# Optimization experiments

Hardware: AMD Instinct MI355X
Metric: run time of the kernel (lower is better)

Reference implementation:

```python
import jax, jax.numpy as jnp
import numpy as np

N = 20000      # nodes
E = 120000     # directed edges (self-loops added in reference, per PyG default)
F_IN = 235
HID = 256
HEADS = 8
NEG_SLOPE = 0.2


def setup_inputs() -> dict:
    key = jax.random.key(0)
    ks = jax.random.split(key, 24)
    p = lambda k, shape: (jax.random.normal(k, shape, jnp.float32) * 0.05)
    inp = {}
    inp["x"] = jax.random.normal(ks[0], (N, F_IN), jnp.float32)
    inp["edge_index"] = jax.random.randint(ks[1], (2, E), 0, N, jnp.int32)
    # input projection
    inp["w_in"] = p(ks[2], (F_IN, HID)); inp["b_in"] = jnp.zeros((HID,), jnp.float32)
    # temporal MLP
    inp["w_t1"] = p(ks[3], (HID, HID)); inp["b_t1"] = jnp.zeros((HID,), jnp.float32)
    inp["w_t2"] = p(ks[4], (HID, HID)); inp["b_t2"] = jnp.zeros((HID,), jnp.float32)
    # GAT layer 1: heads=8, out_per_head=32, concat -> 256
    C1 = HID // HEADS
    inp["w_g1"] = p(ks[5], (HID, HEADS * C1)); inp["a_src1"] = p(ks[6], (HEADS, C1))
    inp["a_dst1"] = p(ks[7], (HEADS, C1)); inp["b_g1"] = jnp.zeros((HEADS * C1,), jnp.float32)
    # GAT layer 2: same shape
    inp["w_g2"] = p(ks[8], (HID, HEADS * C1)); inp["a_src2"] = p(ks[9], (HEADS, C1))
    inp["a_dst2"] = p(ks[10], (HEADS, C1)); inp["b_g2"] = jnp.zeros((HEADS * C1,), jnp.float32)
    # GAT layer 3: heads=8, out_per_head=256, concat -> 2048
    inp["w_g3"] = p(ks[11], (HID, HEADS * HID)); inp["a_src3"] = p(ks[12], (HEADS, HID))
    inp["a_dst3"] = p(ks[13], (HEADS, HID)); inp["b_g3"] = jnp.zeros((HEADS * HID,), jnp.float32)
    # classifier
    inp["w_c1"] = p(ks[14], (2 * HID, HID)); inp["b_c1"] = jnp.zeros((HID,), jnp.float32)
    inp["w_c2"] = p(ks[15], (HID, 2)); inp["b_c2"] = jnp.zeros((2,), jnp.float32)
    return inp


def _gat(x, src, dst, W, a_src, a_dst, b, C):
    """PyG-style GATConv: gather -> per-edge logits -> segment softmax -> scatter-add."""
    h = (x @ W).reshape(-1, HEADS, C)                       # [N, H, C]
    alpha_s = jnp.sum(h * a_src, axis=-1)                   # [N, H]
    alpha_d = jnp.sum(h * a_dst, axis=-1)                   # [N, H]
    e = jax.nn.leaky_relu(alpha_s[src] + alpha_d[dst], NEG_SLOPE)   # [Etot, H]
    m = jax.ops.segment_max(e, dst, num_segments=N)         # [N, H] (self-loops ensure non-empty)
    ex = jnp.exp(e - m[dst])
    den = jax.ops.segment_sum(ex, dst, num_segments=N)
    alpha = ex / (den[dst] + 1e-16)                          # [Etot, H]
    out = jax.ops.segment_sum(alpha[:, :, None] * h[src], dst, num_segments=N)  # [N, H, C]
    return out.reshape(-1, HEADS * C) + b


def reference(x, edge_index, w_in, b_in, w_t1, b_t1, w_t2, b_t2,
              w_g1, a_src1, a_dst1, b_g1, w_g2, a_src2, a_dst2, b_g2,
              w_g3, a_src3, a_dst3, b_g3, w_c1, b_c1, w_c2, b_c2):
    h = jax.nn.elu(x @ w_in + b_in)                          # [N, 256]
    t = jax.nn.relu(h @ w_t1 + b_t1) @ w_t2 + b_t2          # [N, 256] (dropout inactive in eval)
    loop = jnp.arange(N, dtype=edge_index.dtype)
    src = jnp.concatenate([edge_index[0], loop])
    dst = jnp.concatenate([edge_index[1], loop])
    g = jax.nn.elu(_gat(h, src, dst, w_g1, a_src1, a_dst1, b_g1, HID // HEADS))
    g = jax.nn.elu(_gat(g, src, dst, w_g2, a_src2, a_dst2, b_g2, HID // HEADS))
    g = jax.nn.elu(_gat(g, src, dst, w_g3, a_src3, a_dst3, b_g3, HID))  # [N, 2048]
    g = g.reshape(N, HEADS, HID).mean(axis=1)                # [N, 256]
    comb = jnp.concatenate([g, t], axis=-1)                  # [N, 512]
    logits = jax.nn.relu(comb @ w_c1 + b_c1) @ w_c2 + b_c2   # [N, 2]
    return logits
```

## Files before the change

### kernel.cpp

```cpp
#include <hip/hip_runtime.h>
#include <hip/hip_bf16.h>
#include <math.h>


#define HID 256
#define HEADS 8
#define FIN 235

typedef __attribute__((ext_vector_type(8))) short short8;
typedef __attribute__((ext_vector_type(4))) float floatx4;

__device__ __forceinline__ float elu_f(float x) { return x > 0.f ? x : __expf(x) - 1.f; }
__device__ __forceinline__ float bf2f(unsigned short u) {
  return __uint_as_float(((unsigned int)u) << 16);
}
__device__ __forceinline__ unsigned short f2bfu(float f) {
  union { __hip_bfloat16 b; unsigned short u; } c;
  c.b = __float2bfloat16(f);
  return c.u;
}

__global__ void xcvt_k(const float* __restrict__ x, __hip_bfloat16* __restrict__ xb, int M) {
  int id = blockIdx.x * blockDim.x + threadIdx.x;
  if (id >= M * 256) return;
  int m = id >> 8, k = id & 255;
  xb[id] = (k < FIN) ? __float2bfloat16(x[(size_t)m * FIN + k]) : __float2bfloat16(0.f);
}

__global__ void wprep_k(const float* __restrict__ w_in, const float* __restrict__ w_t1,
                        const float* __restrict__ w_g1, const float* __restrict__ w_t2,
                        const float* __restrict__ w_g2, const float* __restrict__ w_c1,
                        const float* __restrict__ w_g3, __hip_bfloat16* __restrict__ wtin,
                        __hip_bfloat16* __restrict__ wtpair, __hip_bfloat16* __restrict__ wtt2,
                        __hip_bfloat16* __restrict__ wtg2, __hip_bfloat16* __restrict__ wtc1,
                        __hip_bfloat16* __restrict__ wtg3s) {
  __shared__ float t[32][33];
  int z = blockIdx.z;
  const float* src;
  __hip_bfloat16* dst;
  int K, Kpad, Nstride;
  if (z == 5) {
    src = w_c1; dst = wtc1; K = 512; Kpad = 512; Nstride = 256;
  } else {
    if (blockIdx.y >= 8) return;
    switch (z) {
      case 0: src = w_in; dst = wtin; K = FIN; Kpad = 256; Nstride = 256; break;
      case 1: src = w_t1; dst = wtpair; K = 256; Kpad = 256; Nstride = 256; break;
      case 2: src = w_g1; dst = wtpair + 256 * 256; K = 256; Kpad = 256; Nstride = 256; break;
      case 3: src = w_t2; dst = wtt2; K = 256; Kpad = 256; Nstride = 256; break;
      case 4: src = w_g2; dst = wtg2; K = 256; Kpad = 256; Nstride = 256; break;
      default: {
        int h = z - 6;
        src = w_g3 + h * 256; dst = wtg3s + h * 256; K = 256; Kpad = 2048; Nstride = 2048;
      }
    }
  }
  int nb = blockIdx.x * 32, kb = blockIdx.y * 32;
  int tx = threadIdx.x, ty = threadIdx.y;
#pragma unroll
  for (int j = 0; j < 32; j += 8) {
    int k = kb + ty + j;
    t[ty + j][tx] = (k < K) ? src[(size_t)k * Nstride + nb + tx] : 0.f;
  }
  __syncthreads();
#pragma unroll
  for (int j = 0; j < 32; j += 8) {
    int n = nb + ty + j;
    int k = kb + tx;
    dst[(size_t)n * Kpad + k] = __float2bfloat16(t[tx][ty + j]);
  }
}

__global__ void count_k(const int* __restrict__ ei, int* __restrict__ deg, int E) {
  int i = blockIdx.x * blockDim.x + threadIdx.x;
  if (i < E) atomicAdd(&deg[ei[E + i]], 1);
}

__global__ void scan_k(const int* __restrict__ deg, int* __restrict__ rp, int n) {
  __shared__ int wsum[16];
  __shared__ int s_carry;
  int tid = threadIdx.x, lane = tid & 63, wid = tid >> 6;
  if (tid == 0) { s_carry = 0; rp[0] = 0; }
  __syncthreads();
  for (int base = 0; base < n; base += 1024) {
    int i = base + tid;
    int x = (i < n) ? (deg[i] + 1) : 0;
#pragma unroll
    for (int off = 1; off < 64; off <<= 1) {
      int y = __shfl_up(x, off);
      if (lane >= off) x += y;
    }
    if (lane == 63) wsum[wid] = x;
    __syncthreads();
    if (wid == 0 && lane < 16) {
      int s = wsum[lane];
#pragma unroll
      for (int off = 1; off < 16; off <<= 1) {
        int y = __shfl_up(s, off);
        if (lane >= off) s += y;
      }
      wsum[lane] = s;
    }
    __syncthreads();
    int offset = s_carry + (wid > 0 ? wsum[wid - 1] : 0);
    if (i < n) rp[i + 1] = offset + x;
    __syncthreads();
    if (tid == 1023) s_carry += wsum[15];
    __syncthreads();
  }
}

__global__ void fill_k(const int* __restrict__ ei, const int* __restrict__ rp,
                       int* __restrict__ fillc, int* __restrict__ colA, int E, int n) {
  int i = blockIdx.x * blockDim.x + threadIdx.x;
  if (i < E) {
    int d = ei[E + i];
    int pos = rp[d] + atomicAdd(&fillc[d], 1);
    colA[pos] = ei[i];
  } else if (i < E + n) {
    int v = i - E;
    int pos = rp[v] + atomicAdd(&fillc[v], 1);
    colA[pos] = v;
  }
}

template <int ACT>
__global__ __launch_bounds__(256) void mgemm64_k(
    const __hip_bfloat16* __restrict__ A, const __hip_bfloat16* __restrict__ Bt,
    const float* __restrict__ bias, __hip_bfloat16* __restrict__ Cb,
    int ldc, int M, int N, int K) {
  __shared__ short As[64 * 40];
  __shared__ short Bs[64 * 40];
  int tid = threadIdx.x;
  int row0 = blockIdx.y * 64, col0 = blockIdx.x * 64;
  int w = tid >> 6, lane = tid & 63;
  int wr = w >> 1, wc = w & 1;
  int quad = lane >> 4, l16 = lane & 15;
  floatx4 zero = {0.f, 0.f, 0.f, 0.f};
  floatx4 acc[2][2];
#pragma unroll
  for (int i = 0; i < 2; i++)
#pragma unroll
    for (int j = 0; j < 2; j++) acc[i][j] = zero;

  int srow = tid >> 2, sq = tid & 3;
  const __hip_bfloat16* Ap = A + (size_t)(row0 + srow) * K + sq * 8;
  const __hip_bfloat16* Bp = Bt + (size_t)(col0 + srow) * K + sq * 8;
  bool aok = (row0 + srow) < M;

  uint4 a1 = make_uint4(0, 0, 0, 0);
  if (aok) a1 = *(const uint4*)(Ap);
  uint4 b1 = *(const uint4*)(Bp);

  for (int k0 = 0; k0 < K; k0 += 32) {
    __syncthreads();
    *(uint4*)&As[srow * 40 + sq * 8] = a1;
    *(uint4*)&Bs[srow * 40 + sq * 8] = b1;
    int kn = k0 + 32;
    if (kn < K) {
      if (aok) a1 = *(const uint4*)(Ap + kn);
      b1 = *(const uint4*)(Bp + kn);
    }
    __syncthreads();
    short8 fa[2], fb[2];
#pragma unroll
    for (int i = 0; i < 2; i++) {
      fa[i] = *(const short8*)&As[(wr * 32 + i * 16 + l16) * 40 + quad * 8];
      fb[i] = *(const short8*)&Bs[(wc * 32 + i * 16 + l16) * 40 + quad * 8];
    }
#pragma unroll
    for (int mi = 0; mi < 2; mi++)
#pragma unroll
      for (int ni = 0; ni < 2; ni++)
        acc[mi][ni] = __builtin_amdgcn_mfma_f32_16x16x32_bf16(fa[mi], fb[ni], acc[mi][ni], 0, 0, 0);
  }

#pragma unroll
  for (int mi = 0; mi < 2; mi++) {
    int rbase = row0 + wr * 32 + mi * 16 + quad * 4;
#pragma unroll
    for (int ni = 0; ni < 2; ni++) {
      int c = col0 + wc * 32 + ni * 16 + l16;
      float bv = bias ? bias[c] : 0.f;
#pragma unroll
      for (int reg = 0; reg < 4; reg++) {
        int rr = rbase + reg;
        if (rr >= M) continue;
        float v = acc[mi][ni][reg] + bv;
        if (ACT == 1) v = fmaxf(v, 0.f);
        if (ACT == 2) v = elu_f(v);
        Cb[(size_t)rr * ldc + c] = __float2bfloat16(v);
      }
    }
  }
}

__global__ __launch_bounds__(256) void mgemm_dual_k(
    const __hip_bfloat16* __restrict__ A, const __hip_bfloat16* __restrict__ Bt,
    const float* __restrict__ bias1, __hip_bfloat16* __restrict__ O1,
    __hip_bfloat16* __restrict__ O2, int M) {
  const int K = 256;
  __shared__ short As[64 * 40];
  __shared__ short Bs[128 * 40];
  int tid = threadIdx.x;
  int row0 = blockIdx.y * 64, col0 = blockIdx.x * 128;
  int w = tid >> 6, lane = tid & 63;
  int wr = w >> 1, wc = w & 1;
  int quad = lane >> 4, l16 = lane & 15;
  floatx4 zero = {0.f, 0.f, 0.f, 0.f};
  floatx4 acc[2][4];
#pragma unroll
  for (int i = 0; i < 2; i++)
#pragma unroll
    for (int j = 0; j < 4; j++) acc[i][j] = zero;

  int srow = tid >> 2, sq = tid & 3;
  const __hip_bfloat16* Ap = A + (size_t)(row0 + srow) * K + sq * 8;
  const __hip_bfloat16* Bp1 = Bt + (size_t)(col0 + srow) * K + sq * 8;
  const __hip_bfloat16* Bp2 = Bt + (size_t)(col0 + 64 + srow) * K + sq * 8;
  bool aok = (row0 + srow) < M;

  uint4 a1 = make_uint4(0, 0, 0, 0);
  if (aok) a1 = *(const uint4*)(Ap);
  uint4 b1 = *(const uint4*)(Bp1);
  uint4 b2 = *(const uint4*)(Bp2);

  for (int k0 = 0; k0 < K; k0 += 32) {
    __syncthreads();
    *(uint4*)&As[srow * 40 + sq * 8] = a1;
    *(uint4*)&Bs[srow * 40 + sq * 8] = b1;
    *(uint4*)&Bs[(64 + srow) * 40 + sq * 8] = b2;
    int kn = k0 + 32;
    if (kn < K) {
      if (aok) a1 = *(const uint4*)(Ap + kn);
      b1 = *(const uint4*)(Bp1 + kn);
      b2 = *(const uint4*)(Bp2 + kn);
    }
    __syncthreads();
    short8 fa[2], fb[4];
#pragma unroll
    for (int i = 0; i < 2; i++)
      fa[i] = *(const short8*)&As[(wr * 32 + i * 16 + l16) * 40 + quad * 8];
#pragma unroll
    for (int i = 0; i < 4; i++)
      fb[i] = *(const short8*)&Bs[(wc * 64 + i * 16 + l16) * 40 + quad * 8];
#pragma unroll
    for (int mi = 0; mi < 2; mi++)
#pragma unroll
      for (int ni = 0; ni < 4; ni++)
        acc[mi][ni] = __builtin_amdgcn_mfma_f32_16x16x32_bf16(fa[mi], fb[ni], acc[mi][ni], 0, 0, 0);
  }

#pragma unroll
  for (int mi = 0; mi < 2; mi++) {
    int rbase = row0 + wr * 32 + mi * 16 + quad * 4;
#pragma unroll
    for (int ni = 0; ni < 4; ni++) {
      int c = col0 + wc * 64 + ni * 16 + l16;
      bool first = c < 256;
      float bv = first ? bias1[c] : 0.f;
      int cc = first ? c : (c - 256);
#pragma unroll
      for (int reg = 0; reg < 4; reg++) {
        int rr = rbase + reg;
        if (rr >= M) continue;
        float v = acc[mi][ni][reg] + bv;
        if (first) v = fmaxf(v, 0.f);
        __hip_bfloat16* dst = first ? O1 : O2;
        dst[(size_t)rr * 256 + cc] = __float2bfloat16(v);
      }
    }
  }
}

__global__ __launch_bounds__(256) void mgemm3_k(
    const __hip_bfloat16* __restrict__ A, const __hip_bfloat16* __restrict__ Bt,
    const float* __restrict__ bias, __hip_bfloat16* __restrict__ comb, int M) {
  const int K = 2048;
  __shared__ short As[64 * 40];
  __shared__ short Bs[64 * 40];
  int tid = threadIdx.x;
  int row0 = blockIdx.y * 64, col0 = blockIdx.x * 64;
  int w = tid >> 6, lane = tid & 63;
  int wr = w >> 1, wc = w & 1;
  int quad = lane >> 4, l16 = lane & 15;
  floatx4 zero = {0.f, 0.f, 0.f, 0.f};
  floatx4 acc[2][2], sum[2][2];
#pragma unroll
  for (int i = 0; i < 2; i++)
#pragma unroll
    for (int j = 0; j < 2; j++) { acc[i][j] = zero; sum[i][j] = zero; }

  int srow = tid >> 2, sq = tid & 3;
  const __hip_bfloat16* Ap = A + (size_t)(row0 + srow) * K + sq * 8;
  const __hip_bfloat16* Bp = Bt + (size_t)(col0 + srow) * K + sq * 8;
  bool aok = (row0 + srow) < M;

  uint4 a1 = make_uint4(0, 0, 0, 0);
  if (aok) a1 = *(const uint4*)(Ap);
  uint4 b1 = *(const uint4*)(Bp);

  for (int k0 = 0; k0 < K; k0 += 32) {
    __syncthreads();
    *(uint4*)&As[srow * 40 + sq * 8] = a1;
    *(uint4*)&Bs[srow * 40 + sq * 8] = b1;
    int kn = k0 + 32;
    if (kn < K) {
      if (aok) a1 = *(const uint4*)(Ap + kn);
      b1 = *(const uint4*)(Bp + kn);
    }
    __syncthreads();
    short8 fa[2], fb[2];
#pragma unroll
    for (int i = 0; i < 2; i++) {
      fa[i] = *(const short8*)&As[(wr * 32 + i * 16 + l16) * 40 + quad * 8];
      fb[i] = *(const short8*)&Bs[(wc * 32 + i * 16 + l16) * 40 + quad * 8];
    }
#pragma unroll
    for (int mi = 0; mi < 2; mi++)
#pragma unroll
      for (int ni = 0; ni < 2; ni++)
        acc[mi][ni] = __builtin_amdgcn_mfma_f32_16x16x32_bf16(fa[mi], fb[ni], acc[mi][ni], 0, 0, 0);
    if (((k0 + 32) & 255) == 0) {
      int h = k0 >> 8;
#pragma unroll
      for (int mi = 0; mi < 2; mi++)
#pragma unroll
        for (int ni = 0; ni < 2; ni++) {
          int c = col0 + wc * 32 + ni * 16 + l16;
          float bv = bias[h * 256 + c];
#pragma unroll
          for (int reg = 0; reg < 4; reg++) {
            sum[mi][ni][reg] += elu_f(acc[mi][ni][reg] + bv);
            acc[mi][ni][reg] = 0.f;
          }
        }
    }
  }

#pragma unroll
  for (int mi = 0; mi < 2; mi++) {
    int rbase = row0 + wr * 32 + mi * 16 + quad * 4;
#pragma unroll
    for (int ni = 0; ni < 2; ni++) {
      int c = col0 + wc * 32 + ni * 16 + l16;
#pragma unroll
      for (int reg = 0; reg < 4; reg++) {
        int rr = rbase + reg;
        if (rr >= M) continue;
        comb[(size_t)rr * 512 + c] = __float2bfloat16(sum[mi][ni][reg] * 0.125f);
      }
    }
  }
}

__global__ __launch_bounds__(256) void mgemm_cls_k(
    const __hip_bfloat16* __restrict__ A, const __hip_bfloat16* __restrict__ Bt,
    const float* __restrict__ bias, const float* __restrict__ w2,
    float* __restrict__ out, int M) {
  const int K = 512;
  __shared__ short As[64 * 40];
  __shared__ short Bs[64 * 40];
  __shared__ float ls[64][2][2];
  int tid = threadIdx.x;
  int row0 = blockIdx.y * 64, col0 = blockIdx.x * 64;
  int w = tid >> 6, lane = tid & 63;
  int wr = w >> 1, wc = w & 1;
  int quad = lane >> 4, l16 = lane & 15;
  floatx4 zero = {0.f, 0.f, 0.f, 0.f};
  floatx4 acc[2][2];
#pragma unroll
  for (int i = 0; i < 2; i++)
#pragma unroll
    for (int j = 0; j < 2; j++) acc[i][j] = zero;

  int srow = tid >> 2, sq = tid & 3;
  const __hip_bfloat16* Ap = A + (size_t)(row0 + srow) * K + sq * 8;
  const __hip_bfloat16* Bp = Bt + (size_t)(col0 + srow) * K + sq * 8;
  bool aok = (row0 + srow) < M;

  uint4 a1 = make_uint4(0, 0, 0, 0);
  if (aok) a1 = *(const uint4*)(Ap);
  uint4 b1 = *(const uint4*)(Bp);

  for (int k0 = 0; k0 < K; k0 += 32) {
    __syncthreads();
    *(uint4*)&As[srow * 40 + sq * 8] = a1;
    *(uint4*)&Bs[srow * 40 + sq * 8] = b1;
    int kn = k0 + 32;
    if (kn < K) {
      if (aok) a1 = *(const uint4*)(Ap + kn);
      b1 = *(const uint4*)(Bp + kn);
    }
    __syncthreads();
    short8 fa[2], fb[2];
#pragma unroll
    for (int i = 0; i < 2; i++) {
      fa[i] = *(const short8*)&As[(wr * 32 + i * 16 + l16) * 40 + quad * 8];
      fb[i] = *(const short8*)&Bs[(wc * 32 + i * 16 + l16) * 40 + quad * 8];
    }
#pragma unroll
    for (int mi = 0; mi < 2; mi++)
#pragma unroll
      for (int ni = 0; ni < 2; ni++)
        acc[mi][ni] = __builtin_amdgcn_mfma_f32_16x16x32_bf16(fa[mi], fb[ni], acc[mi][ni], 0, 0, 0);
  }

  float p[2][4][2];
#pragma unroll
  for (int mi = 0; mi < 2; mi++)
#pragma unroll
    for (int reg = 0; reg < 4; reg++) { p[mi][reg][0] = 0.f; p[mi][reg][1] = 0.f; }
#pragma unroll
  for (int mi = 0; mi < 2; mi++) {
    int rbase = row0 + wr * 32 + mi * 16 + quad * 4;
#pragma unroll
    for (int ni = 0; ni < 2; ni++) {
      int c = col0 + wc * 32 + ni * 16 + l16;
      float bv = bias[c];
      float w20 = w2[c * 2 + 0], w21 = w2[c * 2 + 1];
#pragma unroll
      for (int reg = 0; reg < 4; reg++) {
        if (rbase + reg >= M) continue;
        float v = fmaxf(acc[mi][ni][reg] + bv, 0.f);
        p[mi][reg][0] += v * w20;
        p[mi][reg][1] += v * w21;
      }
    }
  }
#pragma unroll
  for (int off = 1; off < 16; off <<= 1)
#pragma unroll
    for (int mi = 0; mi < 2; mi++)
#pragma unroll
      for (int reg = 0; reg < 4; reg++) {
        p[mi][reg][0] += __shfl_xor(p[mi][reg][0], off);
        p[mi][reg][1] += __shfl_xor(p[mi][reg][1], off);
      }
  if (l16 == 0) {
#pragma unroll
    for (int mi = 0; mi < 2; mi++)
#pragma unroll
      for (int reg = 0; reg < 4; reg++) {
        int rl = wr * 32 + mi * 16 + quad * 4 + reg;
        ls[rl][wc][0] = p[mi][reg][0];
        ls[rl][wc][1] = p[mi][reg][1];
      }
  }
  __syncthreads();
  if (tid < 64) {
    int r = row0 + tid;
    if (r < M) {
      atomicAdd(&out[r * 2 + 0], ls[tid][0][0] + ls[tid][1][0]);
      atomicAdd(&out[r * 2 + 1], ls[tid][0][1] + ls[tid][1][1]);
    }
  }
}

__global__ void initout_k(const float* __restrict__ b, float* __restrict__ out, int M) {
  int i = blockIdx.x * blockDim.x + threadIdx.x;
  if (i < M * 2) out[i] = b[i & 1];
}

__global__ void aproj_k(const float* __restrict__ w_g3, const float* __restrict__ a_s,
                        const float* __restrict__ a_d, float* __restrict__ apj) {
  int idx = blockIdx.x * blockDim.x + threadIdx.x;
  if (idx >= 256 * 16) return;
  int k = idx >> 4, o = idx & 15;
  int h = o >> 1;
  const float* av = (o & 1) ? (a_d + h * 256) : (a_s + h * 256);
  const float* wr = w_g3 + (size_t)k * 2048 + h * 256;
  float s = 0.f;
  for (int c = 0; c < 256; c++) s += wr[c] * av[c];
  apj[idx] = s;
}

__global__ __launch_bounds__(256) void alpha3_k(const __hip_bfloat16* __restrict__ g2,
                                                const float* __restrict__ apj,
                                                float* __restrict__ as_, float* __restrict__ ad_,
                                                int M) {
  int tid = threadIdx.x;
  int nl = tid >> 4, o = tid & 15;
  int n = blockIdx.x * 16 + nl;
  if (n >= M) return;
  const __hip_bfloat16* row = g2 + (size_t)n * 256;
  float s = 0.f;
  for (int c = 0; c < 256; c++) s += __bfloat162float(row[c]) * apj[c * 16 + o];
  if (o & 1) ad_[n * 8 + (o >> 1)] = s;
  else as_[n * 8 + (o >> 1)] = s;
}

__global__ void alpha_small_k(const __hip_bfloat16* __restrict__ hW, const float* __restrict__ a_s,
                              const float* __restrict__ a_d, float* __restrict__ as_,
                              float* __restrict__ ad_, int M) {
  int idx = blockIdx.x * blockDim.x + threadIdx.x;
  if (idx >= M * HEADS) return;
  int h = idx & 7;
  const __hip_bfloat16* row = hW + (size_t)(idx >> 3) * HID + h * 32;
  const float* ws = a_s + h * 32;
  const float* wd = a_d + h * 32;
  float s = 0.f, d = 0.f;
#pragma unroll
  for (int c = 0; c < 32; c++) {
    float v = __bfloat162float(row[c]);
    s += v * ws[c];
    d += v * wd[c];
  }
  as_[idx] = s;
  ad_[idx] = d;
}

__global__ __launch_bounds__(256) void aggf_k(const int* __restrict__ rp,
                                              const int* __restrict__ col,
                                              const __hip_bfloat16* __restrict__ hW,
                                              const float* __restrict__ as_,
                                              const float* __restrict__ ad_,
                                              const float* __restrict__ bias,
                                              __hip_bfloat16* __restrict__ out, int M) {
  int dst = blockIdx.x * 4 + (threadIdx.x >> 6);
  if (dst >= M) return;
  int t = threadIdx.x & 63;
  int h = t >> 3, c = t << 2;
  int beg = rp[dst], end = rp[dst + 1];
  float adv = ad_[dst * 8 + h];
  float m = -3.4e38f;
  for (int i = beg; i < end; i++) {
    float e = as_[col[i] * 8 + h] + adv;
    e = e > 0.f ? e : 0.2f * e;
    m = fmaxf(m, e);
  }
  float den = 0.f;
  float a0 = 0.f, a1 = 0.f, a2 = 0.f, a3 = 0.f;
  for (int i = beg; i < end; i++) {
    int s = col[i];
    float e = as_[s * 8 + h] + adv;
    e = e > 0.f ? e : 0.2f * e;
    float ex = __expf(e - m);
    den += ex;
    union { uint2 u; unsigned short us[4]; } uu;
    uu.u = *(const uint2*)(hW + (size_t)s * HID + c);
    a0 += ex * bf2f(uu.us[0]);
    a1 += ex * bf2f(uu.us[1]);
    a2 += ex * bf2f(uu.us[2]);
    a3 += ex * bf2f(uu.us[3]);
  }
  float inv = 1.f / (den + 1e-16f);
  out[(size_t)dst * HID + c + 0] = __float2bfloat16(elu_f(a0 * inv + bias[c + 0]));
  out[(size_t)dst * HID + c + 1] = __float2bfloat16(elu_f(a1 * inv + bias[c + 1]));
  out[(size_t)dst * HID + c + 2] = __float2bfloat16(elu_f(a2 * inv + bias[c + 2]));
  out[(size_t)dst * HID + c + 3] = __float2bfloat16(elu_f(a3 * inv + bias[c + 3]));
}

__global__ __launch_bounds__(256) void esoft_k(const int* __restrict__ rp,
                                               const int* __restrict__ col,
                                               const float* __restrict__ as_,
                                               const float* __restrict__ ad_,
                                               float* __restrict__ ex,
                                               float* __restrict__ invden, int M) {
  int dst = blockIdx.x * 4 + (threadIdx.x >> 6);
  if (dst >= M) return;
  int lane = threadIdx.x & 63;
  int es = lane >> 3, h = lane & 7;
  int beg = rp[dst], end = rp[dst + 1];
  float adv = ad_[dst * 8 + h];
  float m = -3.4e38f;
  for (int i = beg + es; i < end; i += 8) {
    float e = as_[col[i] * 8 + h] + adv;
    e = e > 0.f ? e : 0.2f * e;
    m = fmaxf(m, e);
  }
  m = fmaxf(m, __shfl_xor(m, 8));
  m = fmaxf(m, __shfl_xor(m, 16));
  m = fmaxf(m, __shfl_xor(m, 32));
  float den = 0.f;
  for (int i = beg + es; i < end; i += 8) {
    float e = as_[col[i] * 8 + h] + adv;
    e = e > 0.f ? e : 0.2f * e;
    float v = __expf(e - m);
    ex[(size_t)i * 8 + h] = v;
    den += v;
  }
  den += __shfl_xor(den, 8);
  den += __shfl_xor(den, 16);
  den += __shfl_xor(den, 32);
  if (es == 0) invden[dst * 8 + h] = 1.f / (den + 1e-16f);
}

__global__ __launch_bounds__(256) void agg3_k(const int* __restrict__ rp,
                                              const int* __restrict__ col,
                                              const __hip_bfloat16* __restrict__ g2,
                                              const float* __restrict__ ex,
                                              const float* __restrict__ invden,
                                              __hip_bfloat16* __restrict__ outA, int M) {
  int dst = blockIdx.x * 2 + (threadIdx.x >> 7);
  if (dst >= M) return;
  int t = threadIdx.x & 127;
  int beg = rp[dst], end = rp[dst + 1];
  float acc0[8] = {}, acc1[8] = {};
  for (int i = beg; i < end; i++) {
    int s = col[i];
    float4 w0 = *(const float4*)(ex + (size_t)i * 8);
    float4 w1 = *(const float4*)(ex + (size_t)i * 8 + 4);
    union { unsigned int u; unsigned short us[2]; } uu;
    uu.u = *(const unsigned int*)(g2 + (size_t)s * 256 + t * 2);
    float v0 = bf2f(uu.us[0]), v1 = bf2f(uu.us[1]);
    acc0[0] += w0.x * v0; acc0[1] += w0.y * v0; acc0[2] += w0.z * v0; acc0[3] += w0.w * v0;
    acc0[4] += w1.x * v0; acc0[5] += w1.y * v0; acc0[6] += w1.z * v0; acc0[7] += w1.w * v0;
    acc1[0] += w0.x * v1; acc1[1] += w0.y * v1; acc1[2] += w0.z * v1; acc1[3] += w0.w * v1;
    acc1[4] += w1.x * v1; acc1[5] += w1.y * v1; acc1[6] += w1.z * v1; acc1[7] += w1.w * v1;
  }
#pragma unroll
  for (int h = 0; h < 8; h++) {
    float inv = invden[dst * 8 + h];
    unsigned int pack = (unsigned int)f2bfu(acc0[h] * inv) |
                        ((unsigned int)f2bfu(acc1[h] * inv) << 16);
    *(unsigned int*)(outA + (size_t)dst * 2048 + h * 256 + t * 2) = pack;
  }
}

extern "C" void kernel_launch(void* const* d_in, const int* in_sizes, int n_in,
                              void* d_out, int out_size, void* d_ws, size_t ws_size,
                              hipStream_t stream) {
  const float* x      = (const float*)d_in[0];
  const int*   ei     = (const int*)d_in[1];
  const float* w_in   = (const float*)d_in[2];
  const float* b_in   = (const float*)d_in[3];
  const float* w_t1   = (const float*)d_in[4];
  const float* b_t1   = (const float*)d_in[5];
  const float* w_t2   = (const float*)d_in[6];
  const float* b_t2   = (const float*)d_in[7];
  const float* w_g1   = (const float*)d_in[8];
  const float* a_src1 = (const float*)d_in[9];
  const float* a_dst1 = (const float*)d_in[10];
  const float* b_g1   = (const float*)d_in[11];
  const float* w_g2   = (const float*)d_in[12];
  const float* a_src2 = (const float*)d_in[13];
  const float* a_dst2 = (const float*)d_in[14];
  const float* b_g2   = (const float*)d_in[15];
  const float* w_g3   = (const float*)d_in[16];
  const float* a_src3 = (const float*)d_in[17];
  const float* a_dst3 = (const float*)d_in[18];
  const float* b_g3   = (const float*)d_in[19];
  const float* w_c1   = (const float*)d_in[20];
  const float* b_c1   = (const float*)d_in[21];
  const float* w_c2   = (const float*)d_in[22];
  const float* b_c2   = (const float*)d_in[23];
  const int M = in_sizes[0] / FIN;
  const int E = in_sizes[1] / 2;
  (void)n_in; (void)out_size; (void)ws_size;

  char* wsb = (char*)d_ws;
  size_t off = 0;
  auto alloc = [&](size_t bytes) {
    void* p = wsb + off;
    off = (off + bytes + 255) & ~(size_t)255;
    return p;
  };
  typedef __hip_bfloat16 bf;
  bf* xb     = (bf*)alloc((size_t)M * 256 * 2);
  bf* wtin   = (bf*)alloc(256 * 256 * 2);
  bf* wtpair = (bf*)alloc(512 * 256 * 2);
  bf* wtt2   = (bf*)alloc(256 * 256 * 2);
  bf* wtg2   = (bf*)alloc(256 * 256 * 2);
  bf* wtg3s  = (bf*)alloc(256 * 2048 * 2);
  bf* wtc1   = (bf*)alloc(256 * 512 * 2);
  bf* actA   = (bf*)alloc((size_t)M * HID * 2);
  bf* actB   = (bf*)alloc((size_t)M * HID * 2);
  bf* hW1    = (bf*)alloc((size_t)M * HID * 2);
  bf* comb   = (bf*)alloc((size_t)M * 2 * HID * 2);
  bf* hWb    = (bf*)alloc((size_t)M * 2048 * 2);
  float* as_ = (float*)alloc((size_t)M * 8 * 4);
  float* ad_ = (float*)alloc((size_t)M * 8 * 4);
  float* apj = (float*)alloc(256 * 16 * 4);
  float* exw = (float*)alloc((size_t)(E + M) * 8 * 4);
  float* ivd = (float*)alloc((size_t)M * 8 * 4);
  int* degfill = (int*)alloc((size_t)2 * M * 4);
  int* deg   = degfill;
  int* fillc = degfill + M;
  int* rp    = (int*)alloc((size_t)(M + 1) * 4);
  int* colA  = (int*)alloc((size_t)(E + M) * 4);

  xcvt_k<<<(M * 256 + 255) / 256, 256, 0, stream>>>(x, xb, M);
  wprep_k<<<dim3(8, 16, 14), dim3(32, 8), 0, stream>>>(
      w_in, w_t1, w_g1, w_t2, w_g2, w_c1, w_g3, wtin, wtpair, wtt2, wtg2, wtc1, wtg3s);
  aproj_k<<<16, 256, 0, stream>>>(w_g3, a_src3, a_dst3, apj);

  hipMemsetAsync(degfill, 0, (size_t)2 * M * 4, stream);
  count_k<<<(E + 255) / 256, 256, 0, stream>>>(ei, deg, E);
  scan_k<<<1, 1024, 0, stream>>>(deg, rp, M);
  fill_k<<<(E + M + 255) / 256, 256, 0, stream>>>(ei, rp, fillc, colA, E, M);

  int eg = (M + 3) / 4;
  int mg = (M + 63) / 64;

  mgemm64_k<2><<<dim3(4, mg), 256, 0, stream>>>(xb, wtin, b_in, actA, HID, M, HID, 256);
  mgemm_dual_k<<<dim3(4, mg), 256, 0, stream>>>(actA, wtpair, b_t1, actB, hW1, M);
  mgemm64_k<0><<<dim3(4, mg), 256, 0, stream>>>(actB, wtt2, b_t2, comb + HID, 2 * HID, M, HID, 256);

  alpha_small_k<<<(M * 8 + 255) / 256, 256, 0, stream>>>(hW1, a_src1, a_dst1, as_, ad_, M);
  aggf_k<<<eg, 256, 0, stream>>>(rp, colA, hW1, as_, ad_, b_g1, actB, M);

  mgemm64_k<0><<<dim3(4, mg), 256, 0, stream>>>(actB, wtg2, nullptr, hW1, HID, M, HID, 256);
  alpha_small_k<<<(M * 8 + 255) / 256, 256, 0, stream>>>(hW1, a_src2, a_dst2, as_, ad_, M);
  aggf_k<<<eg, 256, 0, stream>>>(rp, colA, hW1, as_, ad_, b_g2, actA, M);

  alpha3_k<<<(M + 15) / 16, 256, 0, stream>>>(actA, apj, as_, ad_, M);
  esoft_k<<<eg, 256, 0, stream>>>(rp, colA, as_, ad_, exw, ivd, M);
  agg3_k<<<(M + 1) / 2, 256, 0, stream>>>(rp, colA, actA, exw, ivd, hWb, M);
  mgemm3_k<<<dim3(4, mg), 256, 0, stream>>>(hWb, wtg3s, b_g3, comb, M);

  initout_k<<<(M * 2 + 255) / 256, 256, 0, stream>>>(b_c2, (float*)d_out, M);
  mgemm_cls_k<<<dim3(4, mg), 256, 0, stream>>>(comb, wtc1, b_c1, w_c2, (float*)d_out, M);
}
```

Measured before the change: 446.6 us.

## Widen GEMM tiles to full width, drop atomics, vectorize alpha and aggregation loads

mgemm3 and the classifier GEMM now run 512-thread blocks that each cover a 64-row by 256-column tile. A row's A tile is loaded once instead of four times, and the classifier writes its logits directly with the bias instead of using atomics and a separate init kernel. The a_src3/a_dst3 projection is folded into the weight-prep launch, and alpha3 caches the projection in shared memory and uses 16-byte row loads. agg3 handles four channels per thread with 8-byte loads. In exchange, each block uses more registers and shared memory and there are fewer blocks in flight.

```diff
diff --git a/kernel.cpp b/kernel.cpp
--- a/kernel.cpp
+++ b/kernel.cpp
@@ -30,12 +30,26 @@
 __global__ void wprep_k(const float* __restrict__ w_in, const float* __restrict__ w_t1,
                         const float* __restrict__ w_g1, const float* __restrict__ w_t2,
                         const float* __restrict__ w_g2, const float* __restrict__ w_c1,
-                        const float* __restrict__ w_g3, __hip_bfloat16* __restrict__ wtin,
+                        const float* __restrict__ w_g3, const float* __restrict__ a_s3,
+                        const float* __restrict__ a_d3, __hip_bfloat16* __restrict__ wtin,
                         __hip_bfloat16* __restrict__ wtpair, __hip_bfloat16* __restrict__ wtt2,
                         __hip_bfloat16* __restrict__ wtg2, __hip_bfloat16* __restrict__ wtc1,
-                        __hip_bfloat16* __restrict__ wtg3s) {
+                        __hip_bfloat16* __restrict__ wtg3s, float* __restrict__ apj) {
   __shared__ float t[32][33];
   int z = blockIdx.z;
+  if (z == 14) {
+    int idx = (blockIdx.y * 8 + blockIdx.x) * 256 + threadIdx.y * 32 + threadIdx.x;
+    if (idx < 256 * 16) {
+      int k = idx >> 4, o = idx & 15;
+      int h = o >> 1;
+      const float* av = (o & 1) ? (a_d3 + h * 256) : (a_s3 + h * 256);
+      const float* wr = w_g3 + (size_t)k * 2048 + h * 256;
+      float s = 0.f;
+      for (int c = 0; c < 256; c++) s += wr[c] * av[c];
+      apj[idx] = s;
+    }
+    return;
+  }
   const float* src;
   __hip_bfloat16* dst;
   int K, Kpad, Nstride;
@@ -273,219 +287,188 @@
   }
 }
 
-__global__ __launch_bounds__(256) void mgemm3_k(
+__global__ __launch_bounds__(512) void mgemm3_k(
     const __hip_bfloat16* __restrict__ A, const __hip_bfloat16* __restrict__ Bt,
     const float* __restrict__ bias, __hip_bfloat16* __restrict__ comb, int M) {
   const int K = 2048;
   __shared__ short As[64 * 40];
-  __shared__ short Bs[64 * 40];
+  __shared__ short Bs[256 * 40];
   int tid = threadIdx.x;
-  int row0 = blockIdx.y * 64, col0 = blockIdx.x * 64;
+  int row0 = blockIdx.x * 64;
   int w = tid >> 6, lane = tid & 63;
-  int wr = w >> 1, wc = w & 1;
+  int wr = w & 3, wc = w >> 2;
   int quad = lane >> 4, l16 = lane & 15;
-  floatx4 zero = {0.f, 0.f, 0.f, 0.f};
-  floatx4 acc[2][2], sum[2][2];
-#pragma unroll
-  for (int i = 0; i < 2; i++)
-#pragma unroll
-    for (int j = 0; j < 2; j++) { acc[i][j] = zero; sum[i][j] = zero; }
-
-  int srow = tid >> 2, sq = tid & 3;
-  const __hip_bfloat16* Ap = A + (size_t)(row0 + srow) * K + sq * 8;
-  const __hip_bfloat16* Bp = Bt + (size_t)(col0 + srow) * K + sq * 8;
-  bool aok = (row0 + srow) < M;
+  floatx4 acc[8], sum[8];
+#pragma unroll
+  for (int i = 0; i < 8; i++) {
+    acc[i] = (floatx4){0.f, 0.f, 0.f, 0.f};
+    sum[i] = (floatx4){0.f, 0.f, 0.f, 0.f};
+  }
+
+  bool at = tid < 256;
+  int arow = tid >> 2, achk = (tid & 3) * 8;
+  const __hip_bfloat16* Ap = A + (size_t)(row0 + arow) * K + achk;
+  bool aok = at && (row0 + arow) < M;
+  int brow = tid >> 1, boff = (tid & 1) * 16;
+  const __hip_bfloat16* Bp = Bt + (size_t)brow * K + boff;
 
   uint4 a1 = make_uint4(0, 0, 0, 0);
   if (aok) a1 = *(const uint4*)(Ap);
   uint4 b1 = *(const uint4*)(Bp);
+  uint4 b2 = *(const uint4*)(Bp + 8);
 
   for (int k0 = 0; k0 < K; k0 += 32) {
     __syncthreads();
-    *(uint4*)&As[srow * 40 + sq * 8] = a1;
-    *(uint4*)&Bs[srow * 40 + sq * 8] = b1;
+    if (at) *(uint4*)&As[arow * 40 + achk] = a1;
+    *(uint4*)&Bs[brow * 40 + boff] = b1;
+    *(uint4*)&Bs[brow * 40 + boff + 8] = b2;
     int kn = k0 + 32;
     if (kn < K) {
       if (aok) a1 = *(const uint4*)(Ap + kn);
       b1 = *(const uint4*)(Bp + kn);
-    }
-    __syncthreads();
-    short8 fa[2], fb[2];
-#pragma unroll
-    for (int i = 0; i < 2; i++) {
-      fa[i] = *(const short8*)&As[(wr * 32 + i * 16 + l16) * 40 + quad * 8];
-      fb[i] = *(const short8*)&Bs[(wc * 32 + i * 16 + l16) * 40 + quad * 8];
-    }
-#pragma unroll
-    for (int mi = 0; mi < 2; mi++)
-#pragma unroll
-      for (int ni = 0; ni < 2; ni++)
-        acc[mi][ni] = __builtin_amdgcn_mfma_f32_16x16x32_bf16(fa[mi], fb[ni], acc[mi][ni], 0, 0, 0);
+      b2 = *(const uint4*)(Bp + kn + 8);
+    }
+    __syncthreads();
+    short8 fa = *(const short8*)&As[(wr * 16 + l16) * 40 + quad * 8];
+#pragma unroll
+    for (int ni = 0; ni < 8; ni++) {
+      short8 fb = *(const short8*)&Bs[(wc * 128 + ni * 16 + l16) * 40 + quad * 8];
+      acc[ni] = __builtin_amdgcn_mfma_f32_16x16x32_bf16(fa, fb, acc[ni], 0, 0, 0);
+    }
     if (((k0 + 32) & 255) == 0) {
       int h = k0 >> 8;
 #pragma unroll
-      for (int mi = 0; mi < 2; mi++)
-#pragma unroll
-        for (int ni = 0; ni < 2; ni++) {
-          int c = col0 + wc * 32 + ni * 16 + l16;
-          float bv = bias[h * 256 + c];
-#pragma unroll
-          for (int reg = 0; reg < 4; reg++) {
-            sum[mi][ni][reg] += elu_f(acc[mi][ni][reg] + bv);
-            acc[mi][ni][reg] = 0.f;
-          }
+      for (int ni = 0; ni < 8; ni++) {
+        int c = wc * 128 + ni * 16 + l16;
+        float bv = bias[h * 256 + c];
+#pragma unroll
+        for (int reg = 0; reg < 4; reg++) {
+          sum[ni][reg] += elu_f(acc[ni][reg] + bv);
+          acc[ni][reg] = 0.f;
         }
-    }
-  }
-
-#pragma unroll
-  for (int mi = 0; mi < 2; mi++) {
-    int rbase = row0 + wr * 32 + mi * 16 + quad * 4;
-#pragma unroll
-    for (int ni = 0; ni < 2; ni++) {
-      int c = col0 + wc * 32 + ni * 16 + l16;
-#pragma unroll
-      for (int reg = 0; reg < 4; reg++) {
-        int rr = rbase + reg;
-        if (rr >= M) continue;
-        comb[(size_t)rr * 512 + c] = __float2bfloat16(sum[mi][ni][reg] * 0.125f);
       }
     }
   }
-}
-
-__global__ __launch_bounds__(256) void mgemm_cls_k(
+
+  int rbase = row0 + wr * 16 + quad * 4;
+#pragma unroll
+  for (int ni = 0; ni < 8; ni++) {
+    int c = wc * 128 + ni * 16 + l16;
+#pragma unroll
+    for (int reg = 0; reg < 4; reg++) {
+      int rr = rbase + reg;
+      if (rr >= M) continue;
+      comb[(size_t)rr * 512 + c] = __float2bfloat16(sum[ni][reg] * 0.125f);
+    }
+  }
+}
+
+__global__ __launch_bounds__(512) void mgemm_cls_k(
     const __hip_bfloat16* __restrict__ A, const __hip_bfloat16* __restrict__ Bt,
     const float* __restrict__ bias, const float* __restrict__ w2,
-    float* __restrict__ out, int M) {
+    const float* __restrict__ b2f, float* __restrict__ out, int M) {
   const int K = 512;
   __shared__ short As[64 * 40];
-  __shared__ short Bs[64 * 40];
+  __shared__ short Bs[256 * 40];
   __shared__ float ls[64][2][2];
   int tid = threadIdx.x;
-  int row0 = blockIdx.y * 64, col0 = blockIdx.x * 64;
+  int row0 = blockIdx.x * 64;
   int w = tid >> 6, lane = tid & 63;
-  int wr = w >> 1, wc = w & 1;
+  int wr = w & 3, wc = w >> 2;
   int quad = lane >> 4, l16 = lane & 15;
-  floatx4 zero = {0.f, 0.f, 0.f, 0.f};
-  floatx4 acc[2][2];
-#pragma unroll
-  for (int i = 0; i < 2; i++)
-#pragma unroll
-    for (int j = 0; j < 2; j++) acc[i][j] = zero;
-
-  int srow = tid >> 2, sq = tid & 3;
-  const __hip_bfloat16* Ap = A + (size_t)(row0 + srow) * K + sq * 8;
-  const __hip_bfloat16* Bp = Bt + (size_t)(col0 + srow) * K + sq * 8;
-  bool aok = (row0 + srow) < M;
+  floatx4 acc[8];
+#pragma unroll
+  for (int i = 0; i < 8; i++) acc[i] = (floatx4){0.f, 0.f, 0.f, 0.f};
+
+  bool at = tid < 256;
+  int arow = tid >> 2, achk = (tid & 3) * 8;
+  const __hip_bfloat16* Ap = A + (size_t)(row0 + arow) * K + achk;
+  bool aok = at && (row0 + arow) < M;
+  int brow = tid >> 1, boff = (tid & 1) * 16;
+  const __hip_bfloat16* Bp = Bt + (size_t)brow * K + boff;
 
   uint4 a1 = make_uint4(0, 0, 0, 0);
   if (aok) a1 = *(const uint4*)(Ap);
   uint4 b1 = *(const uint4*)(Bp);
+  uint4 b2 = *(const uint4*)(Bp + 8);
 
   for (int k0 = 0; k0 < K; k0 += 32) {
     __syncthreads();
-    *(uint4*)&As[srow * 40 + sq * 8] = a1;
-    *(uint4*)&Bs[srow * 40 + sq * 8] = b1;
+    if (at) *(uint4*)&As[arow * 40 + achk] = a1;
+    *(uint4*)&Bs[brow * 40 + boff] = b1;
+    *(uint4*)&Bs[brow * 40 + boff + 8] = b2;
     int kn = k0 + 32;
     if (kn < K) {
       if (aok) a1 = *(const uint4*)(Ap + kn);
       b1 = *(const uint4*)(Bp + kn);
-    }
-    __syncthreads();
-    short8 fa[2], fb[2];
-#pragma unroll
-    for (int i = 0; i < 2; i++) {
-      fa[i] = *(const short8*)&As[(wr * 32 + i * 16 + l16) * 40 + quad * 8];
-      fb[i] = *(const short8*)&Bs[(wc * 32 + i * 16 + l16) * 40 + quad * 8];
-    }
-#pragma unroll
-    for (int mi = 0; mi < 2; mi++)
-#pragma unroll
-      for (int ni = 0; ni < 2; ni++)
-        acc[mi][ni] = __builtin_amdgcn_mfma_f32_16x16x32_bf16(fa[mi], fb[ni], acc[mi][ni], 0, 0, 0);
-  }
-
-  float p[2][4][2];
-#pragma unroll
-  for (int mi = 0; mi < 2; mi++)
-#pragma unroll
-    for (int reg = 0; reg < 4; reg++) { p[mi][reg][0] = 0.f; p[mi][reg][1] = 0.f; }
-#pragma unroll
-  for (int mi = 0; mi < 2; mi++) {
-    int rbase = row0 + wr * 32 + mi * 16 + quad * 4;
-#pragma unroll
-    for (int ni = 0; ni < 2; ni++) {
-      int c = col0 + wc * 32 + ni * 16 + l16;
-      float bv = bias[c];
-      float w20 = w2[c * 2 + 0], w21 = w2[c * 2 + 1];
-#pragma unroll
-      for (int reg = 0; reg < 4; reg++) {
-        if (rbase + reg >= M) continue;
-        float v = fmaxf(acc[mi][ni][reg] + bv, 0.f);
-        p[mi][reg][0] += v * w20;
-        p[mi][reg][1] += v * w21;
-      }
+      b2 = *(const uint4*)(Bp + kn + 8);
+    }
+    __syncthreads();
+    short8 fa = *(const short8*)&As[(wr * 16 + l16) * 40 + quad * 8];
+#pragma unroll
+    for (int ni = 0; ni < 8; ni++) {
+      short8 fb = *(const short8*)&Bs[(wc * 128 + ni * 16 + l16) * 40 + quad * 8];
+      acc[ni] = __builtin_amdgcn_mfma_f32_16x16x32_bf16(fa, fb, acc[ni], 0, 0, 0);
+    }
+  }
+
+  float p0[4] = {0.f, 0.f, 0.f, 0.f}, p1[4] = {0.f, 0.f, 0.f, 0.f};
+#pragma unroll
+  for (int ni = 0; ni < 8; ni++) {
+    int c = wc * 128 + ni * 16 + l16;
+    float bv = bias[c];
+    float w20 = w2[c * 2 + 0], w21 = w2[c * 2 + 1];
+#pragma unroll
+    for (int reg = 0; reg < 4; reg++) {
+      float v = fmaxf(acc[ni][reg] + bv, 0.f);
+      p0[reg] += v * w20;
+      p1[reg] += v * w21;
     }
   }
 #pragma unroll
   for (int off = 1; off < 16; off <<= 1)
 #pragma unroll
-    for (int mi = 0; mi < 2; mi++)
-#pragma unroll
-      for (int reg = 0; reg < 4; reg++) {
-        p[mi][reg][0] += __shfl_xor(p[mi][reg][0], off);
-        p[mi][reg][1] += __shfl_xor(p[mi][reg][1], off);
-      }
+    for (int reg = 0; reg < 4; reg++) {
+      p0[reg] += __shfl_xor(p0[reg], off);
+      p1[reg] += __shfl_xor(p1[reg], off);
+    }
   if (l16 == 0) {
 #pragma unroll
-    for (int mi = 0; mi < 2; mi++)
-#pragma unroll
-      for (int reg = 0; reg < 4; reg++) {
-        int rl = wr * 32 + mi * 16 + quad * 4 + reg;
-        ls[rl][wc][0] = p[mi][reg][0];
-        ls[rl][wc][1] = p[mi][reg][1];
-      }
+    for (int reg = 0; reg < 4; reg++) {
+      int rl = wr * 16 + quad * 4 + reg;
+      ls[rl][wc][0] = p0[reg];
+      ls[rl][wc][1] = p1[reg];
+    }
   }
   __syncthreads();
   if (tid < 64) {
     int r = row0 + tid;
     if (r < M) {
-      atomicAdd(&out[r * 2 + 0], ls[tid][0][0] + ls[tid][1][0]);
-      atomicAdd(&out[r * 2 + 1], ls[tid][0][1] + ls[tid][1][1]);
-    }
-  }
-}
-
-__global__ void initout_k(const float* __restrict__ b, float* __restrict__ out, int M) {
-  int i = blockIdx.x * blockDim.x + threadIdx.x;
-  if (i < M * 2) out[i] = b[i & 1];
-}
-
-__global__ void aproj_k(const float* __restrict__ w_g3, const float* __restrict__ a_s,
-                        const float* __restrict__ a_d, float* __restrict__ apj) {
-  int idx = blockIdx.x * blockDim.x + threadIdx.x;
-  if (idx >= 256 * 16) return;
-  int k = idx >> 4, o = idx & 15;
-  int h = o >> 1;
-  const float* av = (o & 1) ? (a_d + h * 256) : (a_s + h * 256);
-  const float* wr = w_g3 + (size_t)k * 2048 + h * 256;
-  float s = 0.f;
-  for (int c = 0; c < 256; c++) s += wr[c] * av[c];
-  apj[idx] = s;
+      out[r * 2 + 0] = ls[tid][0][0] + ls[tid][1][0] + b2f[0];
+      out[r * 2 + 1] = ls[tid][0][1] + ls[tid][1][1] + b2f[1];
+    }
+  }
 }
 
 __global__ __launch_bounds__(256) void alpha3_k(const __hip_bfloat16* __restrict__ g2,
                                                 const float* __restrict__ apj,
                                                 float* __restrict__ as_, float* __restrict__ ad_,
                                                 int M) {
+  __shared__ float sapj[4096];
   int tid = threadIdx.x;
+  for (int i = tid; i < 4096; i += 256) sapj[i] = apj[i];
+  __syncthreads();
   int nl = tid >> 4, o = tid & 15;
   int n = blockIdx.x * 16 + nl;
   if (n >= M) return;
   const __hip_bfloat16* row = g2 + (size_t)n * 256;
   float s = 0.f;
-  for (int c = 0; c < 256; c++) s += __bfloat162float(row[c]) * apj[c * 16 + o];
+  for (int cc = 0; cc < 256; cc += 8) {
+    short8 v8 = *(const short8*)(row + cc);
+#pragma unroll
+    for (int j = 0; j < 8; j++)
+      s += bf2f((unsigned short)v8[j]) * sapj[(cc + j) * 16 + o];
+  }
   if (o & 1) ad_[n * 8 + (o >> 1)] = s;
   else as_[n * 8 + (o >> 1)] = s;
 }
@@ -501,10 +484,14 @@
   const float* wd = a_d + h * 32;
   float s = 0.f, d = 0.f;
 #pragma unroll
-  for (int c = 0; c < 32; c++) {
-    float v = __bfloat162float(row[c]);
-    s += v * ws[c];
-    d += v * wd[c];
+  for (int cc = 0; cc < 32; cc += 8) {
+    short8 v8 = *(const short8*)(row + cc);
+#pragma unroll
+    for (int j = 0; j < 8; j++) {
+      float v = bf2f((unsigned short)v8[j]);
+      s += v * ws[cc + j];
+      d += v * wd[cc + j];
+    }
   }
   as_[idx] = s;
   ad_[idx] = d;
@@ -592,29 +579,37 @@
                                               const float* __restrict__ ex,
                                               const float* __restrict__ invden,
                                               __hip_bfloat16* __restrict__ outA, int M) {
-  int dst = blockIdx.x * 2 + (threadIdx.x >> 7);
+  int dst = blockIdx.x * 4 + (threadIdx.x >> 6);
   if (dst >= M) return;
-  int t = threadIdx.x & 127;
+  int t = threadIdx.x & 63;
   int beg = rp[dst], end = rp[dst + 1];
-  float acc0[8] = {}, acc1[8] = {};
+  float acc[4][8];
+#pragma unroll
+  for (int ch = 0; ch < 4; ch++)
+#pragma unroll
+    for (int h = 0; h < 8; h++) acc[ch][h] = 0.f;
   for (int i = beg; i < end; i++) {
     int s = col[i];
     float4 w0 = *(const float4*)(ex + (size_t)i * 8);
     float4 w1 = *(const float4*)(ex + (size_t)i * 8 + 4);
-    union { unsigned int u; unsigned short us[2]; } uu;
-    uu.u = *(const unsigned int*)(g2 + (size_t)s * 256 + t * 2);
-    float v0 = bf2f(uu.us[0]), v1 = bf2f(uu.us[1]);
-    acc0[0] += w0.x * v0; acc0[1] += w0.y * v0; acc0[2] += w0.z * v0; acc0[3] += w0.w * v0;
-    acc0[4] += w1.x * v0; acc0[5] += w1.y * v0; acc0[6] += w1.z * v0; acc0[7] += w1.w * v0;
-    acc1[0] += w0.x * v1; acc1[1] += w0.y * v1; acc1[2] += w0.z * v1; acc1[3] += w0.w * v1;
-    acc1[4] += w1.x * v1; acc1[5] += w1.y * v1; acc1[6] += w1.z * v1; acc1[7] += w1.w * v1;
+    union { uint2 u; unsigned short us[4]; } uu;
+    uu.u = *(const uint2*)(g2 + (size_t)s * 256 + t * 4);
+#pragma unroll
+    for (int ch = 0; ch < 4; ch++) {
+      float v = bf2f(uu.us[ch]);
+      acc[ch][0] += w0.x * v; acc[ch][1] += w0.y * v;
+      acc[ch][2] += w0.z * v; acc[ch][3] += w0.w * v;
+      acc[ch][4] += w1.x * v; acc[ch][5] += w1.y * v;
+      acc[ch][6] += w1.z * v; acc[ch][7] += w1.w * v;
+    }
   }
 #pragma unroll
   for (int h = 0; h < 8; h++) {
     float inv = invden[dst * 8 + h];
-    unsigned int pack = (unsigned int)f2bfu(acc0[h] * inv) |
-                        ((unsigned int)f2bfu(acc1[h] * inv) << 16);
-    *(unsigned int*)(outA + (size_t)dst * 2048 + h * 256 + t * 2) = pack;
+    union { uint2 u; unsigned short us[4]; } pk;
+#pragma unroll
+    for (int ch = 0; ch < 4; ch++) pk.us[ch] = f2bfu(acc[ch][h] * inv);
+    *(uint2*)(outA + (size_t)dst * 2048 + h * 256 + t * 4) = pk.u;
   }
 }
 
@@ -681,9 +676,9 @@
   int* colA  = (int*)alloc((size_t)(E + M) * 4);
 
   xcvt_k<<<(M * 256 + 255) / 256, 256, 0, stream>>>(x, xb, M);
-  wprep_k<<<dim3(8, 16, 14), dim3(32, 8), 0, stream>>>(
-      w_in, w_t1, w_g1, w_t2, w_g2, w_c1, w_g3, wtin, wtpair, wtt2, wtg2, wtc1, wtg3s);
-  aproj_k<<<16, 256, 0, stream>>>(w_g3, a_src3, a_dst3, apj);
+  wprep_k<<<dim3(8, 16, 15), dim3(32, 8), 0, stream>>>(
+      w_in, w_t1, w_g1, w_t2, w_g2, w_c1, w_g3, a_src3, a_dst3,
+      wtin, wtpair, wtt2, wtg2, wtc1, wtg3s, apj);
 
   hipMemsetAsync(degfill, 0, (size_t)2 * M * 4, stream);
   count_k<<<(E + 255) / 256, 256, 0, stream>>>(ei, deg, E);
@@ -706,9 +701,8 @@
 
   alpha3_k<<<(M + 15) / 16, 256, 0, stream>>>(actA, apj, as_, ad_, M);
   esoft_k<<<eg, 256, 0, stream>>>(rp, colA, as_, ad_, exw, ivd, M);
-  agg3_k<<<(M + 1) / 2, 256, 0, stream>>>(rp, colA, actA, exw, ivd, hWb, M);
-  mgemm3_k<<<dim3(4, mg), 256, 0, stream>>>(hWb, wtg3s, b_g3, comb, M);
-
-  initout_k<<<(M * 2 + 255) / 256, 256, 0, stream>>>(b_c2, (float*)d_out, M);
-  mgemm_cls_k<<<dim3(4, mg), 256, 0, stream>>>(comb, wtc1, b_c1, w_c2, (float*)d_out, M);
-}
+  agg3_k<<<eg, 256, 0, stream>>>(rp, colA, actA, exw, ivd, hWb, M);
+  mgemm3_k<<<mg, 512, 0, stream>>>(hWb, wtg3s, b_g3, comb, M);
+
+  mgemm_cls_k<<<mg, 512, 0, stream>>>(comb, wtc1, b_c1, w_c2, b_c2, (float*)d_out, M);
+}
```

Measured after the change: 435.7 us. 1.03x faster.
